# Kernel optimization log

Hardware: AMD Instinct MI355X
Metric: run time of the kernel (lower is better)

## Reference

```python
import jax, jax.numpy as jnp
import numpy as np

RES, RES_, STRIDE = 28, 14, 2
H, KD, AR = 8, 16, 4
SCALE = KD ** -0.5
EPS = 1e-5


def make_bias_idxs(res=RES, res_=RES_, stride=STRIDE):
    pts = [(i, j) for i in range(res) for j in range(res)]
    pts_ = [(i, j) for i in range(res_) for j in range(res_)]
    offs, idxs = {}, []
    for p1 in pts_:
        for p2 in pts:
            off = (abs(p1[0] * stride - p2[0]), abs(p1[1] * stride - p2[1]))
            if off not in offs:
                offs[off] = len(offs)
            idxs.append(offs[off])
    return np.array(idxs, dtype=np.int32).reshape(len(pts_), len(pts)), len(offs)


def setup_inputs() -> dict:
    key = jax.random.key(0)
    ks = jax.random.split(key, 16)
    idxs, n_off = make_bias_idxs()  # n_off == 784
    B, N, C = 128, RES * RES, 256
    d_kv, d_q, d_p, d_pin = 640, 128, 384, 512
    return {
        "hidden_state": jax.random.normal(ks[0], (B, N, C), jnp.float32),
        "w_kv": jax.random.normal(ks[1], (d_kv, C), jnp.float32) * 0.05,
        "kv_gamma": jax.random.uniform(ks[2], (d_kv,), jnp.float32, 0.5, 1.5),
        "kv_beta": jax.random.normal(ks[3], (d_kv,), jnp.float32) * 0.1,
        "kv_mean": jax.random.normal(ks[4], (d_kv,), jnp.float32) * 0.1,
        "kv_var": jax.random.uniform(ks[5], (d_kv,), jnp.float32, 0.5, 1.5),
        "w_q": jax.random.normal(ks[6], (d_q, C), jnp.float32) * 0.05,
        "q_gamma": jax.random.uniform(ks[7], (d_q,), jnp.float32, 0.5, 1.5),
        "q_beta": jax.random.normal(ks[8], (d_q,), jnp.float32) * 0.1,
        "q_mean": jax.random.normal(ks[9], (d_q,), jnp.float32) * 0.1,
        "q_var": jax.random.uniform(ks[10], (d_q,), jnp.float32, 0.5, 1.5),
        "w_proj": jax.random.normal(ks[11], (d_p, d_pin), jnp.float32) * 0.05,
        "p_gamma": jax.random.uniform(ks[12], (d_p,), jnp.float32, 0.5, 1.5),
        "p_beta": jax.random.normal(ks[13], (d_p,), jnp.float32) * 0.1,
        "p_mean": jax.random.normal(ks[14], (d_p,), jnp.float32) * 0.1,
        "p_var": jax.random.uniform(ks[15], (d_p,), jnp.float32, 0.5, 1.5),
        "attention_biases": jax.random.normal(jax.random.fold_in(key, 99), (H, n_off), jnp.float32),
        "attention_bias_idxs": jnp.asarray(idxs),
    }


def _bn(x, gamma, beta, mean, var):
    # eval-mode BatchNorm1d over last dim
    return (x - mean) * (gamma * jax.lax.rsqrt(var + EPS)) + beta


def _hardswish(x):
    return x * jnp.clip(x + 3.0, 0.0, 6.0) * (1.0 / 6.0)


def reference(hidden_state, w_kv, kv_gamma, kv_beta, kv_mean, kv_var,
              w_q, q_gamma, q_beta, q_mean, q_var,
              w_proj, p_gamma, p_beta, p_mean, p_var,
              attention_biases, attention_bias_idxs):
    B, N, C = hidden_state.shape
    N_ = RES_ * RES_
    # kv: [B, N, 640] -> key [B,H,N,KD], value [B,H,N,AR*KD]
    kv = _bn(hidden_state @ w_kv.T, kv_gamma, kv_beta, kv_mean, kv_var)
    kv = kv.reshape(B, N, H, KD + AR * KD)
    k = jnp.transpose(kv[..., :KD], (0, 2, 1, 3))          # [B,H,N,KD]
    v = jnp.transpose(kv[..., KD:], (0, 2, 1, 3))          # [B,H,N,AR*KD]
    # strided query subsample on the spatial grid
    hs = hidden_state.reshape(B, RES, RES, C)[:, ::STRIDE, ::STRIDE].reshape(B, N_, C)
    q = _bn(hs @ w_q.T, q_gamma, q_beta, q_mean, q_var)
    q = jnp.transpose(q.reshape(B, N_, H, KD), (0, 2, 1, 3))  # [B,H,N_,KD]
    bias = attention_biases[:, attention_bias_idxs]           # [H,N_,N] gathered
    attn = jnp.einsum('bhqd,bhkd->bhqk', q, k) * SCALE + bias
    attn = jax.nn.softmax(attn, axis=-1)
    out = jnp.einsum('bhqk,bhkd->bhqd', attn, v)              # [B,H,N_,AR*KD]
    out = jnp.transpose(out, (0, 2, 1, 3)).reshape(B, N_, H * AR * KD)
    out = _bn(_hardswish(out) @ w_proj.T, p_gamma, p_beta, p_mean, p_var)
    return out
```

## Files before the change

### kernel.cpp

```cpp
#include <hip/hip_runtime.h>

typedef _Float16 f16;
typedef __attribute__((ext_vector_type(2))) _Float16 f16x2;
typedef __attribute__((ext_vector_type(4))) _Float16 f16x4;
typedef __attribute__((ext_vector_type(8))) _Float16 f16x8;
typedef __attribute__((ext_vector_type(4))) float fvec4;
typedef __attribute__((ext_vector_type(4))) float f32x4;
typedef __attribute__((ext_vector_type(16))) float f32x16;
typedef __attribute__((ext_vector_type(4))) unsigned int uint4v;

#define NKEY 784
#define NKEYP 800
#define NQ 196
#define NQP 224

static __device__ __forceinline__ f32x4 mfma16(f16x8 a, f16x8 b, f32x4 c) {
    return __builtin_amdgcn_mfma_f32_16x16x32_f16(a, b, c, 0, 0, 0);
}
static __device__ __forceinline__ f32x16 mfma32(f16x8 a, f16x8 b, f32x16 c) {
    return __builtin_amdgcn_mfma_f32_32x32x16_f16(a, b, c, 0, 0, 0);
}
static __device__ __forceinline__ unsigned pk2(float a, float b) {
    f16x2 t; t[0] = (_Float16)a; t[1] = (_Float16)b;
    return __builtin_bit_cast(unsigned, t);
}
static __device__ __forceinline__ f32x16 z16() {
    f32x16 v;
#pragma unroll
    for (int i = 0; i < 16; ++i) v[i] = 0.f;
    return v;
}

__global__ void prep_scales_all(const float* __restrict__ kg, const float* __restrict__ kb,
                                const float* __restrict__ km, const float* __restrict__ kvv,
                                const float* __restrict__ qg, const float* __restrict__ qb,
                                const float* __restrict__ qm, const float* __restrict__ qv,
                                const float* __restrict__ pg, const float* __restrict__ pb,
                                const float* __restrict__ pm, const float* __restrict__ pv,
                                float* __restrict__ sb) {
    int i = blockIdx.x * 256 + threadIdx.x;
    if (i < 640) {
        float s = kg[i] * rsqrtf(kvv[i] + 1e-5f);
        sb[i] = s; sb[640 + i] = kb[i] - km[i] * s;
    } else if (i < 768) {
        int j = i - 640;
        float s = qg[j] * rsqrtf(qv[j] + 1e-5f);
        sb[1280 + j] = s; sb[1408 + j] = qb[j] - qm[j] * s;
    } else if (i < 1152) {
        int j = i - 768;
        float s = pg[j] * rsqrtf(pv[j] + 1e-5f);
        sb[1536 + j] = s; sb[1920 + j] = pb[j] - pm[j] * s;
    }
}

__global__ void conv_w(const float* __restrict__ wkv, const float* __restrict__ wq,
                       const float* __restrict__ wp, f16* __restrict__ out) {
    int i = blockIdx.x * 256 + threadIdx.x;
    const float* src;
    f16* dst;
    int kc, n, K;
    if (i < 20480)      { int j = i;         kc = j / 640, n = j - kc * 640; src = wkv; dst = out + (size_t)j * 8;            K = 256; }
    else if (i < 24576) { int j = i - 20480; kc = j / 128, n = j - kc * 128; src = wq;  dst = out + 163840 + (size_t)j * 8;   K = 256; }
    else                { int j = i - 24576; kc = j / 384, n = j - kc * 384; src = wp;  dst = out + 196608 + (size_t)j * 8;   K = 512; }
    const float* s = src + (size_t)n * K + kc * 8;
    fvec4 v0 = *(const fvec4*)s;
    fvec4 v1 = *(const fvec4*)(s + 4);
    f16x8 h;
    h[0] = (f16)v0[0]; h[1] = (f16)v0[1]; h[2] = (f16)v0[2]; h[3] = (f16)v0[3];
    h[4] = (f16)v1[0]; h[5] = (f16)v1[1]; h[6] = (f16)v1[2]; h[7] = (f16)v1[3];
    *(f16x8*)dst = h;
}

__global__ void prep_bias(const float* __restrict__ biases, const int* __restrict__ idxs,
                          f16* __restrict__ biasT, int n_off) {
    int tid = blockIdx.x * 256 + threadIdx.x;
    int h = tid / (NQP * NKEYP);
    int rem = tid - h * (NQP * NKEYP);
    int q = rem / NKEYP;
    int key = rem - q * NKEYP;
    float v = 0.f;
    if (q < NQ && key < NKEY) v = biases[h * n_off + idxs[q * NKEY + key]];
    biasT[tid] = (f16)v;
}

template <int MODE>
__global__ __launch_bounds__(MODE == 0 ? 512 : 256) void gemm_lds(
        const void* __restrict__ Ap, const f16x8* __restrict__ Wg,
        const float* __restrict__ sc, const float* __restrict__ sh,
        void* __restrict__ OutA, f16* __restrict__ OutV) {
    constexpr int K     = (MODE == 2) ? 512 : 256;
    constexpr int KS    = K / 32;
    constexpr int TPB   = (MODE == 0) ? 512 : 256;
    constexpr int NT    = (MODE == 0) ? 640 : (MODE == 1 ? 128 : 384);
    constexpr int CHUNK = (MODE == 2) ? 32 : 64;
    constexpr int NCH   = (MODE == 0) ? 5 : (MODE == 1 ? 2 : 6);
    constexpr int NFR   = CHUNK / 16;
    constexpr int UNITS = (K / 8) * CHUNK;
    constexpr int STAGE_R = UNITS / TPB;

    __shared__ f16x8 Wl[UNITS];

    const int t = threadIdx.x;
    const int lane = t & 63, wid = t >> 6;
    const int fr = lane & 15, kg = lane >> 4;
    const int m0 = blockIdx.x * (TPB / 4);
    const int nb0 = blockIdx.y * (NCH * CHUNK);
    const int mrow = m0 + wid * 16 + fr;

    size_t arow;
    if constexpr (MODE == 1) {
        int b = mrow / 196, nn = mrow - b * 196;
        arow = (size_t)b * 784 + (nn / 14) * 56 + (nn % 14) * 2;
    } else {
        arow = (size_t)mrow;
    }
    f16x8 af[KS];
#pragma unroll
    for (int ks = 0; ks < KS; ++ks) {
        if constexpr (MODE == 2) {
            af[ks] = *(const f16x8*)((const f16*)Ap + arow * K + ks * 32 + kg * 8);
        } else {
            const float* a = (const float*)Ap + arow * 256 + ks * 32 + kg * 8;
            fvec4 v0 = *(const fvec4*)a;
            fvec4 v1 = *(const fvec4*)(a + 4);
            f16x8 hv;
            hv[0] = (f16)v0[0]; hv[1] = (f16)v0[1]; hv[2] = (f16)v0[2]; hv[3] = (f16)v0[3];
            hv[4] = (f16)v1[0]; hv[5] = (f16)v1[1]; hv[6] = (f16)v1[2]; hv[7] = (f16)v1[3];
            af[ks] = hv;
        }
    }

    const int rg = kg * 4;
    for (int c = 0; c < NCH; ++c) {
        const int n0c = nb0 + c * CHUNK;
        __syncthreads();
#pragma unroll
        for (int rr = 0; rr < STAGE_R; ++rr) {
            const int idx = rr * TPB + t;
            Wl[idx] = Wg[(size_t)(idx / CHUNK) * NT + n0c + (idx % CHUNK)];
        }
        __syncthreads();

        f32x4 acc[NFR];
#pragma unroll
        for (int j = 0; j < NFR; ++j) acc[j] = (f32x4){0.f, 0.f, 0.f, 0.f};

#pragma unroll
        for (int ks = 0; ks < KS; ++ks) {
            f16x8 bfr[NFR];
#pragma unroll
            for (int nf = 0; nf < NFR; ++nf)
                bfr[nf] = Wl[(ks * 4 + kg) * CHUNK + nf * 16 + fr];
#pragma unroll
            for (int nf = 0; nf < NFR; ++nf)
                acc[nf] = mfma16(af[ks], bfr[nf], acc[nf]);
        }

        const int mbase = m0 + wid * 16 + rg;
#pragma unroll
        for (int nf = 0; nf < NFR; ++nf) {
            const int n = n0c + nf * 16 + fr;
            const float scn = sc[n], shn = sh[n];
            if constexpr (MODE == 0) {
                const int b = mbase / 784;
                const int nn = mbase - b * 784;
                const int hd = n / 80;
                const int cc = n - hd * 80;
                const size_t bh = (size_t)(b * 8 + hd);
                if (cc < 16) {
#pragma unroll
                    for (int r = 0; r < 4; ++r) {
                        float y = acc[nf][r] * scn + shn;
                        ((f16*)OutA)[(bh * NKEYP + nn + r) * 16 + cc] = (f16)y;
                    }
                } else {
                    const int kbk = nn >> 5, off = nn & 31;
                    f16x4 pv;
#pragma unroll
                    for (int r = 0; r < 4; ++r) pv[r] = (f16)(acc[nf][r] * scn + shn);
                    *(f16x4*)(OutV + ((bh * 25 + kbk) * 64 + (cc - 16)) * 32 + off) = pv;
                }
            } else if constexpr (MODE == 1) {
                const int b = mbase / 196;
                const int nn = mbase - b * 196;
                const int hd = n >> 4, cc = n & 15;
                const size_t bh = (size_t)(b * 8 + hd);
#pragma unroll
                for (int r = 0; r < 4; ++r) {
                    float y = acc[nf][r] * scn + shn;
                    ((f16*)OutA)[(bh * NQP + nn + r) * 16 + cc] = (f16)y;
                }
            } else {
#pragma unroll
                for (int r = 0; r < 4; ++r) {
                    float y = acc[nf][r] * scn + shn;
                    ((float*)OutA)[(size_t)(mbase + r) * 384 + n] = y;
                }
            }
        }
    }
}

__global__ __launch_bounds__(448) void attn_fused(const f16* __restrict__ kb,
                                                  const f16* __restrict__ vtb,
                                                  const f16* __restrict__ qw,
                                                  const f16* __restrict__ biasT,
                                                  f16* __restrict__ ao) {
    const int bh = blockIdx.x;
    const int b = bh >> 3, h = bh & 7;
    const int wid = threadIdx.x >> 6;
    const int lane = threadIdx.x & 63;
    const int l31 = lane & 31;
    const int hh = lane >> 5;
    const int q0 = wid * 32;

    const f16* kp = kb + (size_t)bh * (NKEYP * 16);
    const f16* vp = vtb + (size_t)bh * (25 * 64 * 32) + l31 * 32;
    const f16x8 bq = *(const f16x8*)(qw + ((size_t)bh * NQP + q0 + l31) * 16 + hh * 8);
    const f16* bbq = biasT + ((size_t)h * NQP + (q0 + l31)) * NKEYP;

    float mrun = -1e30f;
    float lsum = 0.f;
    f32x16 o0 = z16(), o1 = z16();

    for (int key0 = 0; key0 < NKEY; key0 += 32) {
        f16x8 ak = *(const f16x8*)(kp + (size_t)(key0 + l31) * 16 + hh * 8);
        f32x16 s = mfma32(ak, bq, z16());
        const bool tail = (key0 + 32) > NKEY;
        f16x4 bw[4];
#pragma unroll
        for (int g = 0; g < 4; ++g)
            bw[g] = *(const f16x4*)(bbq + key0 + g * 8 + hh * 4);
        float p[16];
        float cmax = -3.0e38f;
#pragma unroll
        for (int r = 0; r < 16; ++r) {
            const int cr = (r & 3) + ((r >> 2) << 3) + (hh << 2);
            float sv = s[r] * 0.25f + (float)bw[r >> 2][r & 3];
            if (tail && (key0 + cr) >= NKEY) sv = -1e30f;
            p[r] = sv;
            cmax = fmaxf(cmax, sv);
        }
        cmax = fmaxf(cmax, __shfl_xor(cmax, 32));
        if (__any(cmax > mrun + 8.f)) {
            float mnew = fmaxf(mrun, cmax);
            float f = __expf(mrun - mnew);
            mrun = mnew;
            lsum *= f;
#pragma unroll
            for (int r = 0; r < 16; ++r) {
                const int cr = (r & 3) + ((r >> 2) << 3) + (hh << 2);
                float fr2 = __shfl(f, cr);
                o0[r] *= fr2;
                o1[r] *= fr2;
            }
        }
        float psum = 0.f;
#pragma unroll
        for (int r = 0; r < 16; ++r) {
            p[r] = __expf(p[r] - mrun);
            psum += p[r];
        }
        lsum += psum;
        unsigned g0l = pk2(p[0], p[1]),   g0h = pk2(p[2], p[3]);
        unsigned g1l = pk2(p[4], p[5]),   g1h = pk2(p[6], p[7]);
        unsigned g2l = pk2(p[8], p[9]),   g2h = pk2(p[10], p[11]);
        unsigned g3l = pk2(p[12], p[13]), g3h = pk2(p[14], p[15]);
        __builtin_amdgcn_s_setprio(1);
        const f16* vkb = vp + (key0 >> 5) * (64 * 32);
#pragma unroll
        for (int sH = 0; sH < 2; ++sH) {
            unsigned self_lo = sH ? (hh ? g3l : g2l) : (hh ? g1l : g0l);
            unsigned self_hi = sH ? (hh ? g3h : g2h) : (hh ? g1h : g0h);
            unsigned tx_lo   = sH ? (hh ? g2l : g3l) : (hh ? g0l : g1l);
            unsigned tx_hi   = sH ? (hh ? g2h : g3h) : (hh ? g0h : g1h);
            unsigned rx_lo = __shfl_xor(tx_lo, 32);
            unsigned rx_hi = __shfl_xor(tx_hi, 32);
            uint4v w;
            w[0] = hh ? rx_lo : self_lo;
            w[1] = hh ? rx_hi : self_hi;
            w[2] = hh ? self_lo : rx_lo;
            w[3] = hh ? self_hi : rx_hi;
            f16x8 pa = __builtin_bit_cast(f16x8, w);
            const f16* vrow = vkb + sH * 16 + hh * 8;
            f16x8 bv0 = *(const f16x8*)(vrow);
            f16x8 bv1 = *(const f16x8*)(vrow + 32 * 32);
            o0 = mfma32(pa, bv0, o0);
            o1 = mfma32(pa, bv1, o1);
        }
        __builtin_amdgcn_s_setprio(0);
    }
    lsum += __shfl_xor(lsum, 32);
    const float inv = 1.0f / lsum;
#pragma unroll
    for (int r = 0; r < 16; ++r) {
        const int cr = (r & 3) + ((r >> 2) << 3) + (hh << 2);
        const float iq = __shfl(inv, cr);
        const int qg = q0 + cr;
        if (qg < NQ) {
            float v0 = o0[r] * iq, v1 = o1[r] * iq;
            float h0 = v0 * fminf(fmaxf(v0 + 3.f, 0.f), 6.f) * (1.f / 6.f);
            float h1 = v1 * fminf(fmaxf(v1 + 3.f, 0.f), 6.f) * (1.f / 6.f);
            f16* dst = ao + ((size_t)b * NQ + qg) * 512 + h * 64 + l31;
            dst[0] = (f16)h0;
            dst[32] = (f16)h1;
        }
    }
}

extern "C" void kernel_launch(void* const* d_in, const int* in_sizes, int n_in,
                              void* d_out, int out_size, void* d_ws, size_t ws_size,
                              hipStream_t stream) {
    (void)n_in; (void)out_size; (void)ws_size;
    const float* hidden = (const float*)d_in[0];
    const float* w_kv   = (const float*)d_in[1];
    const float* w_q    = (const float*)d_in[6];
    const float* w_p    = (const float*)d_in[11];
    const float* biases = (const float*)d_in[16];
    const int*   idxs   = (const int*)d_in[17];
    const int n_off = in_sizes[16] / 8;

    char* ws = (char*)d_ws;
    const size_t OFF_K  = 0;
    const size_t OFF_V  = 26214400;
    const size_t OFF_Q  = 131072000;
    const size_t OFF_AO = 138412032;
    const size_t OFF_BT = 164102144;
    const size_t OFF_W  = 166969344;
    const size_t OFF_SC = 167755776;
    f16*   kbuf  = (f16*)(ws + OFF_K);
    f16*   vbuf  = (f16*)(ws + OFF_V);
    f16*   qbuf  = (f16*)(ws + OFF_Q);
    f16*   aobuf = (f16*)(ws + OFF_AO);
    f16*   btbuf = (f16*)(ws + OFF_BT);
    f16*   wf16  = (f16*)(ws + OFF_W);
    float* scbuf = (float*)(ws + OFF_SC);

    prep_scales_all<<<5, 256, 0, stream>>>(
        (const float*)d_in[2], (const float*)d_in[3], (const float*)d_in[4], (const float*)d_in[5],
        (const float*)d_in[7], (const float*)d_in[8], (const float*)d_in[9], (const float*)d_in[10],
        (const float*)d_in[12], (const float*)d_in[13], (const float*)d_in[14], (const float*)d_in[15],
        scbuf);
    conv_w<<<192, 256, 0, stream>>>(w_kv, w_q, w_p, wf16);
    prep_bias<<<5600, 256, 0, stream>>>(biases, idxs, btbuf, n_off);
    hipMemsetAsync(qbuf, 0, (size_t)1024 * NQP * 16 * 2, stream);
    gemm_lds<0><<<dim3(784, 2), 512, 0, stream>>>(hidden, (const f16x8*)wf16, scbuf, scbuf + 640, kbuf, vbuf);
    gemm_lds<1><<<dim3(392, 1), 256, 0, stream>>>(hidden, (const f16x8*)(wf16 + 163840), scbuf + 1280, scbuf + 1408, qbuf, nullptr);
    attn_fused<<<1024, 448, 0, stream>>>(kbuf, vbuf, qbuf, btbuf, aobuf);
    gemm_lds<2><<<dim3(392, 2), 256, 0, stream>>>(aobuf, (const f16x8*)(wf16 + 196608), scbuf + 1536, scbuf + 1920, d_out, nullptr);
}
```

Before: 243.4 us.

## Double-buffer LDS weight tiles in projection GEMMs with register prefetch

```diff
diff --git a/kernel.cpp b/kernel.cpp
--- a/kernel.cpp
+++ b/kernel.cpp
@@ -84,26 +84,25 @@
 }
 
 template <int MODE>
-__global__ __launch_bounds__(MODE == 0 ? 512 : 256) void gemm_lds(
+__global__ __launch_bounds__(256) void gemm_db(
         const void* __restrict__ Ap, const f16x8* __restrict__ Wg,
         const float* __restrict__ sc, const float* __restrict__ sh,
         void* __restrict__ OutA, f16* __restrict__ OutV) {
     constexpr int K     = (MODE == 2) ? 512 : 256;
     constexpr int KS    = K / 32;
-    constexpr int TPB   = (MODE == 0) ? 512 : 256;
+    constexpr int CHUNK = (MODE == 2) ? 16 : 32;
+    constexpr int NFR   = CHUNK / 16;
     constexpr int NT    = (MODE == 0) ? 640 : (MODE == 1 ? 128 : 384);
-    constexpr int CHUNK = (MODE == 2) ? 32 : 64;
-    constexpr int NCH   = (MODE == 0) ? 5 : (MODE == 1 ? 2 : 6);
-    constexpr int NFR   = CHUNK / 16;
+    constexpr int NCH   = (MODE == 0) ? 10 : (MODE == 1 ? 4 : 12);
     constexpr int UNITS = (K / 8) * CHUNK;
-    constexpr int STAGE_R = UNITS / TPB;
-
-    __shared__ f16x8 Wl[UNITS];
+    constexpr int SR    = UNITS / 256;
+
+    __shared__ f16x8 Wl[2][UNITS];
 
     const int t = threadIdx.x;
     const int lane = t & 63, wid = t >> 6;
     const int fr = lane & 15, kg = lane >> 4;
-    const int m0 = blockIdx.x * (TPB / 4);
+    const int m0 = blockIdx.x * 64;
     const int nb0 = blockIdx.y * (NCH * CHUNK);
     const int mrow = m0 + wid * 16 + fr;
 
@@ -130,27 +129,36 @@
         }
     }
 
+#pragma unroll
+    for (int rr = 0; rr < SR; ++rr) {
+        const int idx = rr * 256 + t;
+        Wl[0][idx] = Wg[(size_t)(idx / CHUNK) * NT + nb0 + (idx % CHUNK)];
+    }
+    __syncthreads();
+
     const int rg = kg * 4;
+    int cur = 0;
     for (int c = 0; c < NCH; ++c) {
         const int n0c = nb0 + c * CHUNK;
-        __syncthreads();
-#pragma unroll
-        for (int rr = 0; rr < STAGE_R; ++rr) {
-            const int idx = rr * TPB + t;
-            Wl[idx] = Wg[(size_t)(idx / CHUNK) * NT + n0c + (idx % CHUNK)];
-        }
-        __syncthreads();
+
+        f16x8 nx0, nx1, nx2, nx3;
+        if (c + 1 < NCH) {
+            const int n0n = n0c + CHUNK;
+            nx0 = Wg[(size_t)((0 * 256 + t) / CHUNK) * NT + n0n + ((0 * 256 + t) % CHUNK)];
+            nx1 = Wg[(size_t)((1 * 256 + t) / CHUNK) * NT + n0n + ((1 * 256 + t) % CHUNK)];
+            nx2 = Wg[(size_t)((2 * 256 + t) / CHUNK) * NT + n0n + ((2 * 256 + t) % CHUNK)];
+            nx3 = Wg[(size_t)((3 * 256 + t) / CHUNK) * NT + n0n + ((3 * 256 + t) % CHUNK)];
+        }
 
         f32x4 acc[NFR];
 #pragma unroll
         for (int j = 0; j < NFR; ++j) acc[j] = (f32x4){0.f, 0.f, 0.f, 0.f};
-
 #pragma unroll
         for (int ks = 0; ks < KS; ++ks) {
             f16x8 bfr[NFR];
 #pragma unroll
             for (int nf = 0; nf < NFR; ++nf)
-                bfr[nf] = Wl[(ks * 4 + kg) * CHUNK + nf * 16 + fr];
+                bfr[nf] = Wl[cur][(ks * 4 + kg) * CHUNK + nf * 16 + fr];
 #pragma unroll
             for (int nf = 0; nf < NFR; ++nf)
                 acc[nf] = mfma16(af[ks], bfr[nf], acc[nf]);
@@ -197,6 +205,15 @@
                     ((float*)OutA)[(size_t)(mbase + r) * 384 + n] = y;
                 }
             }
+        }
+
+        if (c + 1 < NCH) {
+            Wl[cur ^ 1][0 * 256 + t] = nx0;
+            Wl[cur ^ 1][1 * 256 + t] = nx1;
+            Wl[cur ^ 1][2 * 256 + t] = nx2;
+            Wl[cur ^ 1][3 * 256 + t] = nx3;
+            __syncthreads();
+            cur ^= 1;
         }
     }
 }
@@ -344,8 +361,8 @@
     conv_w<<<192, 256, 0, stream>>>(w_kv, w_q, w_p, wf16);
     prep_bias<<<5600, 256, 0, stream>>>(biases, idxs, btbuf, n_off);
     hipMemsetAsync(qbuf, 0, (size_t)1024 * NQP * 16 * 2, stream);
-    gemm_lds<0><<<dim3(784, 2), 512, 0, stream>>>(hidden, (const f16x8*)wf16, scbuf, scbuf + 640, kbuf, vbuf);
-    gemm_lds<1><<<dim3(392, 1), 256, 0, stream>>>(hidden, (const f16x8*)(wf16 + 163840), scbuf + 1280, scbuf + 1408, qbuf, nullptr);
+    gemm_db<0><<<dim3(1568, 2), 256, 0, stream>>>(hidden, (const f16x8*)wf16, scbuf, scbuf + 640, kbuf, vbuf);
+    gemm_db<1><<<dim3(392, 1), 256, 0, stream>>>(hidden, (const f16x8*)(wf16 + 163840), scbuf + 1280, scbuf + 1408, qbuf, nullptr);
     attn_fused<<<1024, 448, 0, stream>>>(kbuf, vbuf, qbuf, btbuf, aobuf);
-    gemm_lds<2><<<dim3(392, 2), 256, 0, stream>>>(aobuf, (const f16x8*)(wf16 + 196608), scbuf + 1536, scbuf + 1920, d_out, nullptr);
-}
+    gemm_db<2><<<dim3(392, 2), 256, 0, stream>>>(aobuf, (const f16x8*)(wf16 + 196608), scbuf + 1536, scbuf + 1920, d_out, nullptr);
+}
```

Result: faster. 226.6 us (-6.9%).
